# Kernel tuning notes

Hardware: AMD Instinct MI355X
Metric: run time of the kernel (lower is better)

The kernel has to match this reference:

```python
import jax, jax.numpy as jnp
import numpy as np

N_CHANNELS = 1024
N_HEADS = 16
SEQ = 2048
BATCH = 2


def setup_inputs() -> dict:
    key = jax.random.key(0)
    k1, k2, k3 = jax.random.split(key, 3)
    x = jax.random.normal(k1, (BATCH, SEQ, N_CHANNELS), dtype=jnp.float32)
    qkv_w = jax.random.normal(k2, (3 * N_CHANNELS, N_CHANNELS), dtype=jnp.float32) * 0.02
    qkv_b = jnp.zeros((3 * N_CHANNELS,), dtype=jnp.float32)
    proj_w = jax.random.normal(k3, (N_CHANNELS, N_CHANNELS), dtype=jnp.float32) * 0.02
    proj_b = jnp.zeros((N_CHANNELS,), dtype=jnp.float32)
    return {"x": x, "qkv_w": qkv_w, "qkv_b": qkv_b, "proj_w": proj_w, "proj_b": proj_b}


def reference(x, qkv_w, qkv_b, proj_w, proj_b):
    bs, t, c = x.shape
    h = N_HEADS
    hd = c // h
    scale = hd ** (-0.5)
    # qkv projection: torch Linear is x @ W^T + b
    qkv = x @ qkv_w.T + qkv_b  # [B, T, 3C]
    qkv = qkv.reshape(bs, t, 3, h, hd)
    q, k, v = qkv[:, :, 0], qkv[:, :, 1], qkv[:, :, 2]  # each [B, T, H, hd]
    logits = jnp.einsum('bthc,bshc->bhts', q, k) * scale  # [B, H, T, T]
    # causal mask: log(tril(ones)) -> 0 below diag, -inf above
    causal = jnp.tril(jnp.ones((t, t), dtype=bool))
    logits = jnp.where(causal[None, None], logits, -jnp.inf)
    attn = jax.nn.softmax(logits, axis=-1)
    out = jnp.einsum('bhts,bshc->bthc', attn, v).reshape(bs, t, c)
    out = out @ proj_w.T + proj_b
    return out
```

## Files before the change

kernel.cpp:

```cpp
#include <hip/hip_runtime.h>

typedef __bf16 bf16x8 __attribute__((ext_vector_type(8)));
typedef float f32x4 __attribute__((ext_vector_type(4)));

__device__ inline ushort f2bf(float f) {
    unsigned u = __builtin_bit_cast(unsigned, f);
    unsigned r = (u + 0x7FFFu + ((u >> 16) & 1u)) >> 16;
    return (ushort)r;
}
__device__ inline float bf2f(ushort u) {
    unsigned x = ((unsigned)u) << 16;
    return __builtin_bit_cast(float, x);
}
__device__ inline uint4 pack8(const float* f) {
    uint4 r;
    r.x = (unsigned)f2bf(f[0]) | ((unsigned)f2bf(f[1]) << 16);
    r.y = (unsigned)f2bf(f[2]) | ((unsigned)f2bf(f[3]) << 16);
    r.z = (unsigned)f2bf(f[4]) | ((unsigned)f2bf(f[5]) << 16);
    r.w = (unsigned)f2bf(f[6]) | ((unsigned)f2bf(f[7]) << 16);
    return r;
}

#define MFMA_BF16(a, b, c) __builtin_amdgcn_mfma_f32_16x16x32_bf16(a, b, c, 0, 0, 0)
#define GLDS(g, l) __builtin_amdgcn_global_load_lds( \
    (const __attribute__((address_space(1))) void*)(g), \
    (__attribute__((address_space(3))) void*)(l), 16, 0, 0)

#define QSCALE 0.1803368801111437f

__global__ void detect_dtype(const ushort* __restrict__ x, int* __restrict__ flag) {
    const int lane = threadIdx.x;
    const ushort u = x[lane];
    const int e = (u >> 7) & 0xFF;
    const bool plausible = (e >= 100 && e <= 150) || ((u & 0x7FFF) == 0);
    const unsigned long long m = __ballot(plausible);
    if (lane == 0) flag[0] = (__popcll(m) >= 50) ? 1 : 0;
}

__global__ __launch_bounds__(256) void convert3(
    const void* __restrict__ s0, ushort* __restrict__ d0,
    const void* __restrict__ s1, ushort* __restrict__ d1,
    const void* __restrict__ s2, ushort* __restrict__ d2,
    const int* __restrict__ flag)
{
    const int i = blockIdx.x * 256 + threadIdx.x;
    const void* s; ushort* d; int off;
    if (i < 524288)      { s = s0; d = d0; off = i; }
    else if (i < 917504) { s = s1; d = d1; off = i - 524288; }
    else                 { s = s2; d = d2; off = i - 917504; }
    if (flag[0]) {
        ((uint4*)d)[off] = ((const uint4*)s)[off];
    } else {
        const float4* f = (const float4*)s + off * 2;
        float fa[8];
        *(float4*)&fa[0] = f[0];
        *(float4*)&fa[4] = f[1];
        ((uint4*)d)[off] = pack8(fa);
    }
}

template <int MODE>
__global__ __launch_bounds__(256) void gemm128(
    const ushort* __restrict__ A, const ushort* __restrict__ B,
    const void* __restrict__ biasp, void* __restrict__ outD,
    ushort* __restrict__ outQ, ushort* __restrict__ outK, ushort* __restrict__ outV,
    const int* __restrict__ flag, int N, int K)
{
    __shared__ __align__(16) ushort SMEM[2][128 * 64];
    ushort* As = SMEM[0];
    ushort* Bs = SMEM[1];

    const int isb = flag[0];
    const int tid = threadIdx.x;
    const int w = tid >> 6;
    const int lane = tid & 63;
    const int l15 = lane & 15;
    const int quad = lane >> 4;
    const int m0 = blockIdx.x * 128;
    const int n0 = blockIdx.y * 128;
    const int wr = (w & 1) * 64;
    const int wc = (w >> 1) * 64;

    f32x4 acc[4][4] = {};

    for (int k0 = 0; k0 < K; k0 += 64) {
        __syncthreads();
#pragma unroll
        for (int j = 0; j < 4; j++) {
            const int r0 = w * 32 + j * 8;
            const int row = r0 + (lane >> 3);
            const int gcol = ((lane & 7) ^ (row & 7)) * 8;
            GLDS(A + (size_t)(m0 + row) * K + k0 + gcol, As + r0 * 64);
            GLDS(B + (size_t)(n0 + row) * K + k0 + gcol, Bs + r0 * 64);
        }
        __syncthreads();

        bf16x8 af[4][2], bf[4][2];
#pragma unroll
        for (int i = 0; i < 4; i++)
#pragma unroll
            for (int kk = 0; kk < 2; kk++) {
                const int ra = wr + i * 16 + l15;
                const int rb = wc + i * 16 + l15;
                const int ua = ((kk * 4 + quad) ^ (ra & 7)) * 8;
                const int ub = ((kk * 4 + quad) ^ (rb & 7)) * 8;
                af[i][kk] = *(const bf16x8*)&As[ra * 64 + ua];
                bf[i][kk] = *(const bf16x8*)&Bs[rb * 64 + ub];
            }
#pragma unroll
        for (int kk = 0; kk < 2; kk++)
#pragma unroll
            for (int mi = 0; mi < 4; mi++)
#pragma unroll
                for (int ni = 0; ni < 4; ni++)
                    acc[mi][ni] = MFMA_BF16(af[mi][kk], bf[ni][kk], acc[mi][ni]);
    }

    if (MODE == 0 && (n0 >> 10) == 2) {
        __syncthreads();
        ushort* Ct = &SMEM[0][0];
#pragma unroll
        for (int mi = 0; mi < 4; mi++)
#pragma unroll
            for (int ni = 0; ni < 4; ni++)
#pragma unroll
                for (int r = 0; r < 4; r++) {
                    const int m_loc = wr + mi * 16 + quad * 4 + r;
                    const int n_loc = wc + ni * 16 + l15;
                    const int n = n0 + n_loc;
                    const float bias_n = isb ? bf2f(((const ushort*)biasp)[n])
                                             : ((const float*)biasp)[n];
                    Ct[n_loc * 128 + (m_loc ^ ((n_loc & 15) << 3))] =
                        f2bf(acc[mi][ni][r] + bias_n);
                }
        __syncthreads();
#pragma unroll
        for (int i = 0; i < 8; i++) {
            const int vi = tid + i * 256;
            const int n_loc = vi >> 4;
            const int mblk = vi & 15;
            const uint4 val = *(const uint4*)&Ct[n_loc * 128 + ((mblk ^ (n_loc & 15)) << 3)];
            const int m = m0 + mblk * 8;
            const int b = m >> 11, t = m & 2047;
            const int c = (n0 + n_loc) & 1023;
            const int h = c >> 6, d = c & 63;
            *(uint4*)&outV[((size_t)(b * 16 + h) * 64 + d) * 2048 + t] = val;
        }
        return;
    }

#pragma unroll
    for (int mi = 0; mi < 4; mi++)
#pragma unroll
        for (int ni = 0; ni < 4; ni++)
#pragma unroll
            for (int r = 0; r < 4; r++) {
                const int m = m0 + wr + mi * 16 + quad * 4 + r;
                const int n = n0 + wc + ni * 16 + l15;
                const float bias_n = isb ? bf2f(((const ushort*)biasp)[n])
                                         : ((const float*)biasp)[n];
                float v = acc[mi][ni][r] + bias_n;
                if (MODE == 0) {
                    const int which = n >> 10, c = n & 1023;
                    const int h = c >> 6, d = c & 63;
                    const int b = m >> 11, t = m & 2047;
                    if (which == 0) {
                        outQ[(((size_t)(b * 16 + h)) * 2048 + t) * 64 + d] = f2bf(v * QSCALE);
                    } else {
                        outK[(((size_t)(b * 16 + h)) * 2048 + t) * 64 + d] = f2bf(v);
                    }
                } else {
                    if (isb) ((ushort*)outD)[(size_t)m * N + n] = f2bf(v);
                    else     ((float*)outD)[(size_t)m * N + n] = v;
                }
            }
}

__global__ __launch_bounds__(256) void attn2(
    const ushort* __restrict__ Q, const ushort* __restrict__ K,
    const ushort* __restrict__ Vt, ushort* __restrict__ O)
{
    __shared__ __align__(16) ushort KV[2][2][64 * 64];
    __shared__ __align__(16) __bf16 Ps[4][16 * 72];

    const int bh = blockIdx.x;
    const int qt = 31 - blockIdx.y;
    const int q0 = qt * 64;
    const int tid = threadIdx.x;
    const int w = tid >> 6;
    const int lane = tid & 63;
    const int l15 = lane & 15;
    const int quad = lane >> 4;

    auto stage = [&](int kt, int b) {
        const int t0 = kt * 64;
#pragma unroll
        for (int j = 0; j < 2; j++) {
            const int r0 = w * 16 + j * 8;
            const int row = r0 + (lane >> 3);
            const int gcol = ((lane & 7) ^ (row & 7)) * 8;
            GLDS(K + ((size_t)bh * 2048 + t0 + row) * 64 + gcol, &KV[b][0][r0 * 64]);
            GLDS(Vt + ((size_t)bh * 64 + row) * 2048 + t0 + gcol, &KV[b][1][r0 * 64]);
        }
    };

    const ushort* qbase = Q + ((size_t)bh * 2048 + q0 + w * 16 + l15) * 64;
    bf16x8 qf0 = *(const bf16x8*)(qbase + quad * 8);
    bf16x8 qf1 = *(const bf16x8*)(qbase + 32 + quad * 8);

    bf16x8 ones;
#pragma unroll
    for (int j = 0; j < 8; j++) ones[j] = (__bf16)1.0f;

    f32x4 oacc[4] = {};
    f32x4 lacc = {};

    stage(0, 0);

    for (int kt = 0; kt <= qt; kt++) {
        __syncthreads();
        if (kt < qt) stage(kt + 1, (kt + 1) & 1);

        const ushort* Ks = &KV[kt & 1][0][0];
        const ushort* Vs = &KV[kt & 1][1][0];
        const int t0 = kt * 64;

        f32x4 sacc[4] = {};
#pragma unroll
        for (int cb = 0; cb < 4; cb++) {
            const int rr = cb * 16 + l15;
            bf16x8 b0 = *(const bf16x8*)&Ks[rr * 64 + ((quad ^ (rr & 7)) * 8)];
            bf16x8 b1 = *(const bf16x8*)&Ks[rr * 64 + (((4 + quad) ^ (rr & 7)) * 8)];
            sacc[cb] = MFMA_BF16(qf0, b0, sacc[cb]);
            sacc[cb] = MFMA_BF16(qf1, b1, sacc[cb]);
        }

        __bf16* pw = &Ps[w][0];
        __builtin_amdgcn_wave_barrier();
        if (kt == qt) {
#pragma unroll
            for (int cb = 0; cb < 4; cb++)
#pragma unroll
                for (int r = 0; r < 4; r++) {
                    const int col = t0 + cb * 16 + l15;
                    const int row = q0 + w * 16 + quad * 4 + r;
                    const float x = (col > row) ? -1e30f : sacc[cb][r];
                    pw[(quad * 4 + r) * 72 + cb * 16 + l15] =
                        (__bf16)__builtin_exp2f(x);
                }
        } else {
#pragma unroll
            for (int cb = 0; cb < 4; cb++)
#pragma unroll
                for (int r = 0; r < 4; r++)
                    pw[(quad * 4 + r) * 72 + cb * 16 + l15] =
                        (__bf16)__builtin_exp2f(sacc[cb][r]);
        }
        __builtin_amdgcn_s_waitcnt(0xC07F);
        __builtin_amdgcn_wave_barrier();

#pragma unroll
        for (int kc = 0; kc < 2; kc++) {
            bf16x8 afr = *(const bf16x8*)&pw[l15 * 72 + kc * 32 + quad * 8];
#pragma unroll
            for (int cb = 0; cb < 4; cb++) {
                const int rr = cb * 16 + l15;
                bf16x8 bfr = *(const bf16x8*)&Vs[rr * 64 + (((kc * 4 + quad) ^ (rr & 7)) * 8)];
                oacc[cb] = MFMA_BF16(afr, bfr, oacc[cb]);
            }
            lacc = MFMA_BF16(afr, ones, lacc);
        }
    }

    const int b = bh >> 4, h = bh & 15;
#pragma unroll
    for (int r = 0; r < 4; r++) {
        const float inv = 1.0f / lacc[r];
        const int row = q0 + w * 16 + quad * 4 + r;
#pragma unroll
        for (int cb = 0; cb < 4; cb++) {
            const int col = h * 64 + cb * 16 + l15;
            O[((size_t)b * 2048 + row) * 1024 + col] = f2bf(oacc[cb][r] * inv);
        }
    }
}

extern "C" void kernel_launch(void* const* d_in, const int* in_sizes, int n_in,
                              void* d_out, int out_size, void* d_ws, size_t ws_size,
                              hipStream_t stream) {
    const void* x      = d_in[0];
    const void* qkv_w  = d_in[1];
    const void* qkv_b  = d_in[2];
    const void* proj_w = d_in[3];
    const void* proj_b = d_in[4];

    int* flag = (int*)d_ws;
    ushort* XbOb  = (ushort*)d_ws + 16;
    ushort* Wqkv  = XbOb + 4194304;
    ushort* Wproj = Wqkv + 3145728;
    ushort* Qb    = Wproj + 1048576;
    ushort* Kb    = Qb + 4194304;
    ushort* Vt    = Kb + 4194304;

    detect_dtype<<<1, 64, 0, stream>>>((const ushort*)x, flag);
    convert3<<<4096, 256, 0, stream>>>(x, XbOb, qkv_w, Wqkv, proj_w, Wproj, flag);
    gemm128<0><<<dim3(32, 24), 256, 0, stream>>>(XbOb, Wqkv, qkv_b, nullptr,
                                                 Qb, Kb, Vt, flag, 3072, 1024);
    attn2<<<dim3(32, 32), 256, 0, stream>>>(Qb, Kb, Vt, XbOb);
    gemm128<1><<<dim3(32, 8), 256, 0, stream>>>(XbOb, Wproj, proj_b, d_out,
                                                nullptr, nullptr, nullptr, flag, 1024, 1024);
}
```

Baseline: 224.0 us.

## Stage GEMM epilogues through LDS for vectorized stores and drop dtype detection

Removes the runtime dtype-detection kernel and the flag branches, hardcoding fp32 inputs and output. The Q/K epilogue and the projection epilogue now stage results through padded LDS tiles, so each thread writes 16-byte vectors instead of scattered 2- or 4-byte stores. The V transpose path switches from an XOR swizzle to padding. This cuts one launch and improves store coalescing, at the cost of extra LDS round-trips and barriers and the loss of support for bf16 inputs.

```diff
diff --git a/kernel.cpp b/kernel.cpp
--- a/kernel.cpp
+++ b/kernel.cpp
@@ -7,10 +7,6 @@
     unsigned u = __builtin_bit_cast(unsigned, f);
     unsigned r = (u + 0x7FFFu + ((u >> 16) & 1u)) >> 16;
     return (ushort)r;
-}
-__device__ inline float bf2f(ushort u) {
-    unsigned x = ((unsigned)u) << 16;
-    return __builtin_bit_cast(float, x);
 }
 __device__ inline uint4 pack8(const float* f) {
     uint4 r;
@@ -26,51 +22,36 @@
     (const __attribute__((address_space(1))) void*)(g), \
     (__attribute__((address_space(3))) void*)(l), 16, 0, 0)
 
-#define QSCALE 0.1803368801111437f
-
-__global__ void detect_dtype(const ushort* __restrict__ x, int* __restrict__ flag) {
-    const int lane = threadIdx.x;
-    const ushort u = x[lane];
-    const int e = (u >> 7) & 0xFF;
-    const bool plausible = (e >= 100 && e <= 150) || ((u & 0x7FFF) == 0);
-    const unsigned long long m = __ballot(plausible);
-    if (lane == 0) flag[0] = (__popcll(m) >= 50) ? 1 : 0;
-}
+#define QSCALE 0.18033688011112042f
 
 __global__ __launch_bounds__(256) void convert3(
-    const void* __restrict__ s0, ushort* __restrict__ d0,
-    const void* __restrict__ s1, ushort* __restrict__ d1,
-    const void* __restrict__ s2, ushort* __restrict__ d2,
-    const int* __restrict__ flag)
+    const float* __restrict__ s0, ushort* __restrict__ d0,
+    const float* __restrict__ s1, ushort* __restrict__ d1,
+    const float* __restrict__ s2, ushort* __restrict__ d2)
 {
     const int i = blockIdx.x * 256 + threadIdx.x;
-    const void* s; ushort* d; int off;
+    const float* s; ushort* d; int off;
     if (i < 524288)      { s = s0; d = d0; off = i; }
     else if (i < 917504) { s = s1; d = d1; off = i - 524288; }
     else                 { s = s2; d = d2; off = i - 917504; }
-    if (flag[0]) {
-        ((uint4*)d)[off] = ((const uint4*)s)[off];
-    } else {
-        const float4* f = (const float4*)s + off * 2;
-        float fa[8];
-        *(float4*)&fa[0] = f[0];
-        *(float4*)&fa[4] = f[1];
-        ((uint4*)d)[off] = pack8(fa);
-    }
+    const float4* f = (const float4*)s + off * 2;
+    float fa[8];
+    *(float4*)&fa[0] = f[0];
+    *(float4*)&fa[4] = f[1];
+    ((uint4*)d)[off] = pack8(fa);
 }
 
 template <int MODE>
 __global__ __launch_bounds__(256) void gemm128(
     const ushort* __restrict__ A, const ushort* __restrict__ B,
-    const void* __restrict__ biasp, void* __restrict__ outD,
+    const float* __restrict__ bias, float* __restrict__ outD,
     ushort* __restrict__ outQ, ushort* __restrict__ outK, ushort* __restrict__ outV,
-    const int* __restrict__ flag, int N, int K)
+    int N, int K)
 {
-    __shared__ __align__(16) ushort SMEM[2][128 * 64];
-    ushort* As = SMEM[0];
-    ushort* Bs = SMEM[1];
-
-    const int isb = flag[0];
+    __shared__ __align__(16) ushort SMEM[17408];
+    ushort* As = SMEM;
+    ushort* Bs = SMEM + 8192;
+
     const int tid = threadIdx.x;
     const int w = tid >> 6;
     const int lane = tid & 63;
@@ -116,64 +97,93 @@
                     acc[mi][ni] = MFMA_BF16(af[mi][kk], bf[ni][kk], acc[mi][ni]);
     }
 
-    if (MODE == 0 && (n0 >> 10) == 2) {
-        __syncthreads();
-        ushort* Ct = &SMEM[0][0];
-#pragma unroll
-        for (int mi = 0; mi < 4; mi++)
-#pragma unroll
-            for (int ni = 0; ni < 4; ni++)
-#pragma unroll
-                for (int r = 0; r < 4; r++) {
-                    const int m_loc = wr + mi * 16 + quad * 4 + r;
-                    const int n_loc = wc + ni * 16 + l15;
-                    const int n = n0 + n_loc;
-                    const float bias_n = isb ? bf2f(((const ushort*)biasp)[n])
-                                             : ((const float*)biasp)[n];
-                    Ct[n_loc * 128 + (m_loc ^ ((n_loc & 15) << 3))] =
-                        f2bf(acc[mi][ni][r] + bias_n);
-                }
+    if (MODE == 0) {
+        const int which = n0 >> 10;
+        ushort* Ct = SMEM;
+        __syncthreads();
+        if (which == 2) {
+#pragma unroll
+            for (int mi = 0; mi < 4; mi++)
+#pragma unroll
+                for (int ni = 0; ni < 4; ni++)
+#pragma unroll
+                    for (int r = 0; r < 4; r++) {
+                        const int m_loc = wr + mi * 16 + quad * 4 + r;
+                        const int n_loc = wc + ni * 16 + l15;
+                        Ct[n_loc * 136 + m_loc] =
+                            f2bf(acc[mi][ni][r] + bias[n0 + n_loc]);
+                    }
+            __syncthreads();
+            const int b = m0 >> 11;
+#pragma unroll
+            for (int i = 0; i < 8; i++) {
+                const int vi = tid + i * 256;
+                const int n_loc = vi >> 4, mblk = vi & 15;
+                const uint4 val = *(const uint4*)&Ct[n_loc * 136 + mblk * 8];
+                const int t = (m0 & 2047) + mblk * 8;
+                const int c = (n0 + n_loc) & 1023;
+                const int h = c >> 6, d = c & 63;
+                *(uint4*)&outV[((size_t)(b * 16 + h) * 64 + d) * 2048 + t] = val;
+            }
+        } else {
+            const float qs = (which == 0) ? QSCALE : 1.0f;
+#pragma unroll
+            for (int mi = 0; mi < 4; mi++)
+#pragma unroll
+                for (int ni = 0; ni < 4; ni++)
+#pragma unroll
+                    for (int r = 0; r < 4; r++) {
+                        const int m_loc = wr + mi * 16 + quad * 4 + r;
+                        const int n_loc = wc + ni * 16 + l15;
+                        Ct[m_loc * 136 + n_loc] =
+                            f2bf((acc[mi][ni][r] + bias[n0 + n_loc]) * qs);
+                    }
+            __syncthreads();
+            ushort* outP = (which == 0) ? outQ : outK;
+            const int hb = (n0 & 1023) >> 6;
+            const int b = m0 >> 11;
+#pragma unroll
+            for (int i = 0; i < 8; i++) {
+                const int vi = tid + i * 256;
+                const int m_loc = vi >> 4, u = vi & 15;
+                const uint4 val = *(const uint4*)&Ct[m_loc * 136 + u * 8];
+                const int t = (m0 & 2047) + m_loc;
+                const int h = hb + (u >> 3);
+                const int d8 = (u & 7) * 8;
+                *(uint4*)&outP[((size_t)(b * 16 + h)) * 131072 + (size_t)t * 64 + d8] = val;
+            }
+        }
+        return;
+    }
+
+    float* Cf = (float*)SMEM;
+#pragma unroll
+    for (int cch = 0; cch < 2; cch++) {
+        __syncthreads();
+        if ((wc >> 6) == cch) {
+#pragma unroll
+            for (int mi = 0; mi < 4; mi++)
+#pragma unroll
+                for (int ni = 0; ni < 4; ni++)
+#pragma unroll
+                    for (int r = 0; r < 4; r++) {
+                        const int m_loc = wr + mi * 16 + quad * 4 + r;
+                        const int nl = ni * 16 + l15;
+                        Cf[m_loc * 68 + nl] =
+                            acc[mi][ni][r] + bias[n0 + cch * 64 + nl];
+                    }
+        }
         __syncthreads();
 #pragma unroll
         for (int i = 0; i < 8; i++) {
             const int vi = tid + i * 256;
-            const int n_loc = vi >> 4;
-            const int mblk = vi & 15;
-            const uint4 val = *(const uint4*)&Ct[n_loc * 128 + ((mblk ^ (n_loc & 15)) << 3)];
-            const int m = m0 + mblk * 8;
-            const int b = m >> 11, t = m & 2047;
-            const int c = (n0 + n_loc) & 1023;
-            const int h = c >> 6, d = c & 63;
-            *(uint4*)&outV[((size_t)(b * 16 + h) * 64 + d) * 2048 + t] = val;
-        }
-        return;
-    }
-
-#pragma unroll
-    for (int mi = 0; mi < 4; mi++)
-#pragma unroll
-        for (int ni = 0; ni < 4; ni++)
-#pragma unroll
-            for (int r = 0; r < 4; r++) {
-                const int m = m0 + wr + mi * 16 + quad * 4 + r;
-                const int n = n0 + wc + ni * 16 + l15;
-                const float bias_n = isb ? bf2f(((const ushort*)biasp)[n])
-                                         : ((const float*)biasp)[n];
-                float v = acc[mi][ni][r] + bias_n;
-                if (MODE == 0) {
-                    const int which = n >> 10, c = n & 1023;
-                    const int h = c >> 6, d = c & 63;
-                    const int b = m >> 11, t = m & 2047;
-                    if (which == 0) {
-                        outQ[(((size_t)(b * 16 + h)) * 2048 + t) * 64 + d] = f2bf(v * QSCALE);
-                    } else {
-                        outK[(((size_t)(b * 16 + h)) * 2048 + t) * 64 + d] = f2bf(v);
-                    }
-                } else {
-                    if (isb) ((ushort*)outD)[(size_t)m * N + n] = f2bf(v);
-                    else     ((float*)outD)[(size_t)m * N + n] = v;
-                }
-            }
+            const int m_loc = vi >> 4, u = vi & 15;
+            const float4 val = *(const float4*)&Cf[m_loc * 68 + u * 4];
+            const int m = m0 + m_loc;
+            const int n = n0 + cch * 64 + u * 4;
+            *(float4*)&outD[(size_t)m * N + n] = val;
+        }
+    }
 }
 
 __global__ __launch_bounds__(256) void attn2(
@@ -288,13 +298,12 @@
 extern "C" void kernel_launch(void* const* d_in, const int* in_sizes, int n_in,
                               void* d_out, int out_size, void* d_ws, size_t ws_size,
                               hipStream_t stream) {
-    const void* x      = d_in[0];
-    const void* qkv_w  = d_in[1];
-    const void* qkv_b  = d_in[2];
-    const void* proj_w = d_in[3];
-    const void* proj_b = d_in[4];
-
-    int* flag = (int*)d_ws;
+    const float* x      = (const float*)d_in[0];
+    const float* qkv_w  = (const float*)d_in[1];
+    const float* qkv_b  = (const float*)d_in[2];
+    const float* proj_w = (const float*)d_in[3];
+    const float* proj_b = (const float*)d_in[4];
+
     ushort* XbOb  = (ushort*)d_ws + 16;
     ushort* Wqkv  = XbOb + 4194304;
     ushort* Wproj = Wqkv + 3145728;
@@ -302,11 +311,10 @@
     ushort* Kb    = Qb + 4194304;
     ushort* Vt    = Kb + 4194304;
 
-    detect_dtype<<<1, 64, 0, stream>>>((const ushort*)x, flag);
-    convert3<<<4096, 256, 0, stream>>>(x, XbOb, qkv_w, Wqkv, proj_w, Wproj, flag);
+    convert3<<<4096, 256, 0, stream>>>(x, XbOb, qkv_w, Wqkv, proj_w, Wproj);
     gemm128<0><<<dim3(32, 24), 256, 0, stream>>>(XbOb, Wqkv, qkv_b, nullptr,
-                                                 Qb, Kb, Vt, flag, 3072, 1024);
+                                                 Qb, Kb, Vt, 3072, 1024);
     attn2<<<dim3(32, 32), 256, 0, stream>>>(Qb, Kb, Vt, XbOb);
-    gemm128<1><<<dim3(32, 8), 256, 0, stream>>>(XbOb, Wproj, proj_b, d_out,
-                                                nullptr, nullptr, nullptr, flag, 1024, 1024);
-}
+    gemm128<1><<<dim3(32, 8), 256, 0, stream>>>(XbOb, Wproj, proj_b, (float*)d_out,
+                                                nullptr, nullptr, nullptr, 1024, 1024);
+}
```

New measurement: 201.8 us. 1.11x faster.
